# Kernel optimization log

Hardware: AMD Instinct MI355X
Metric: run time of the kernel (lower is better)

The kernel has to match this reference:

```python
import jax, jax.numpy as jnp
import numpy as np

B, L, H2 = 64, 1024, 1024  # batch, src_len, 2*hidden_size


def setup_inputs() -> dict:
    key = jax.random.key(0)
    k1, k2, k3, k4, k5, k6 = jax.random.split(key, 6)
    s = 0.02
    return {
        "s_t_hat": jax.random.normal(k1, (B, H2), jnp.float32),
        "encoder_outputs": jax.random.normal(k2, (B, L, H2), jnp.float32),
        "encoder_features": jax.random.normal(k3, (B * L, H2), jnp.float32),
        "encoder_pad_mask": jnp.ones((B, L), jnp.float32),
        "W": jax.random.normal(k4, (H2, H2), jnp.float32) * s,  # W_s_b_attn.weight
        "b": jax.random.normal(k5, (H2,), jnp.float32) * s,     # W_s_b_attn.bias
        "v": jax.random.normal(k6, (H2,), jnp.float32) * s,     # v.weight (no bias)
    }


def reference(s_t_hat, encoder_outputs, encoder_features, encoder_pad_mask, W, b, v):
    Bb, Ll, Hh = encoder_outputs.shape
    # decoder_features = W_s_b_attn(s_t_hat), broadcast over src positions
    dec = s_t_hat @ W.T + b                                # [B, H2]
    attn_feats = encoder_features.reshape(Bb, Ll, Hh) + dec[:, None, :]
    e = jnp.tanh(attn_feats) @ v                            # [B, L]
    attn_dist = jax.nn.softmax(e, axis=1) * encoder_pad_mask
    attn_dist = attn_dist / attn_dist.sum(axis=1, keepdims=True)
    c_t = jnp.einsum('bl,blh->bh', attn_dist, encoder_outputs)  # [B, H2]
    return c_t
```

## Files before the change

### kernel.cpp

```cpp
#include <hip/hip_runtime.h>

#define H2    1024
#define LSRC  1024
#define BATCH 64
#define NCH   32
#define CH    32
#define RPW   8

__device__ __forceinline__ float fast_tanh(float x) {
  float e2 = __expf(2.0f * x);
  return 1.0f - 2.0f * __builtin_amdgcn_rcpf(e2 + 1.0f);
}

__global__ __launch_bounds__(256) void dec_kernel(
    const float* __restrict__ s, const float* __restrict__ W,
    const float* __restrict__ bias, float* __restrict__ dec) {
  const int KT = 128;
  __shared__ float s_lds[BATCH][KT + 1];
  __shared__ float w_lds[16][KT];
  const int t  = threadIdx.x;
  const int h0 = blockIdx.x * 16;
  const int bi = t & 63;
  const int hg = t >> 6;
  float acc[4] = {0.f, 0.f, 0.f, 0.f};
  for (int k0 = 0; k0 < H2; k0 += KT) {
    __syncthreads();
    for (int idx = t; idx < BATCH * KT; idx += 256) {
      int r = idx >> 7, c = idx & (KT - 1);
      s_lds[r][c] = s[r * H2 + k0 + c];
    }
    for (int idx = t; idx < 16 * KT; idx += 256) {
      int r = idx >> 7, c = idx & (KT - 1);
      w_lds[r][c] = W[(h0 + r) * H2 + k0 + c];
    }
    __syncthreads();
    for (int k = 0; k < KT; ++k) {
      float sv = s_lds[bi][k];
#pragma unroll
      for (int j = 0; j < 4; ++j) acc[j] += sv * w_lds[hg + 4 * j][k];
    }
  }
#pragma unroll
  for (int j = 0; j < 4; ++j) {
    int h = h0 + hg + 4 * j;
    dec[bi * H2 + h] = acc[j] + bias[h];
  }
}

__global__ __launch_bounds__(256) void fused_kernel(
    const float* __restrict__ ef, const float* __restrict__ eo,
    const float* __restrict__ dec, const float* __restrict__ v,
    const float* __restrict__ mask, float* __restrict__ part,
    float* __restrict__ sums) {
  __shared__ float dv_lds[2 * H2];
  __shared__ float a_lds[CH];
  __shared__ float wpsum[4];
  const int t    = threadIdx.x;
  const int lane = t & 63;
  const int wave = t >> 6;
  const int lc   = blockIdx.x;
  const int b    = blockIdx.y;
  const int l0   = lc * CH;

  ((float4*)dv_lds)[t]       = ((const float4*)(dec + (size_t)b * H2))[t];
  ((float4*)dv_lds)[256 + t] = ((const float4*)v)[t];
  __syncthreads();

  const float4* efb = (const float4*)(ef) + ((size_t)b * LSRC + l0) * 256;
  float lsum = 0.f;
#pragma unroll
  for (int i = 0; i < RPW; ++i) {
    const int rl = wave + 4 * i;
    const float4* row = efb + (size_t)rl * 256;
    float sum = 0.f;
#pragma unroll
    for (int j = 0; j < 4; ++j) {
      float4 x  = row[lane + 64 * j];
      float4 dj = ((const float4*)dv_lds)[lane + 64 * j];
      float4 vj = ((const float4*)dv_lds)[256 + lane + 64 * j];
      sum += fast_tanh(x.x + dj.x) * vj.x;
      sum += fast_tanh(x.y + dj.y) * vj.y;
      sum += fast_tanh(x.z + dj.z) * vj.z;
      sum += fast_tanh(x.w + dj.w) * vj.w;
    }
#pragma unroll
    for (int off = 32; off; off >>= 1) sum += __shfl_xor(sum, off);
    float mk = mask[b * LSRC + l0 + rl];
    if (lane == 0) {
      float w = __expf(fminf(sum, 80.f)) * mk;
      a_lds[rl] = w;
      lsum += w;
    }
  }
  if (lane == 0) wpsum[wave] = lsum;
  __syncthreads();
  if (t == 0) sums[b * NCH + lc] = wpsum[0] + wpsum[1] + wpsum[2] + wpsum[3];

  const float4* eob = (const float4*)(eo) + ((size_t)b * LSRC + l0) * 256;
  float4 acc = {0.f, 0.f, 0.f, 0.f};
#pragma unroll 8
  for (int l = 0; l < CH; ++l) {
    float  a = a_lds[l];
    float4 x = eob[(size_t)l * 256 + t];
    acc.x += a * x.x; acc.y += a * x.y; acc.z += a * x.z; acc.w += a * x.w;
  }
  ((float4*)(part) + (size_t)(lc * BATCH + b) * 256)[t] = acc;
}

__global__ __launch_bounds__(256) void reduce_kernel(
    const float* __restrict__ part, const float* __restrict__ sums,
    float* __restrict__ out) {
  const int b = blockIdx.x, t = threadIdx.x;
  float Z = 0.f;
#pragma unroll
  for (int lc = 0; lc < NCH; ++lc) Z += sums[b * NCH + lc];
  float inv = 1.0f / Z;
  float4 s = {0.f, 0.f, 0.f, 0.f};
#pragma unroll
  for (int lc = 0; lc < NCH; ++lc) {
    float4 x = ((const float4*)(part) + (size_t)(lc * BATCH + b) * 256)[t];
    s.x += x.x; s.y += x.y; s.z += x.z; s.w += x.w;
  }
  float4 o = {s.x * inv, s.y * inv, s.z * inv, s.w * inv};
  ((float4*)(out) + (size_t)b * 256)[t] = o;
}

extern "C" void kernel_launch(void* const* d_in, const int* in_sizes, int n_in,
                              void* d_out, int out_size, void* d_ws, size_t ws_size,
                              hipStream_t stream) {
  const float* s_t_hat  = (const float*)d_in[0];
  const float* enc_out  = (const float*)d_in[1];
  const float* enc_feat = (const float*)d_in[2];
  const float* mask     = (const float*)d_in[3];
  const float* W        = (const float*)d_in[4];
  const float* bias     = (const float*)d_in[5];
  const float* v        = (const float*)d_in[6];
  float* out = (float*)d_out;

  float* dec  = (float*)d_ws;
  float* sums = dec + BATCH * H2;
  float* part = sums + BATCH * NCH;

  dec_kernel<<<H2 / 16, 256, 0, stream>>>(s_t_hat, W, bias, dec);
  fused_kernel<<<dim3(NCH, BATCH), 256, 0, stream>>>(
      enc_feat, enc_out, dec, v, mask, part, sums);
  reduce_kernel<<<BATCH, 256, 0, stream>>>(part, sums, out);
}
```

Measured before the change: 153.6 us.

## Reassign score computation: each thread owns a hidden slice across all rows with transpose-reduce

The score phase now has each thread hold a fixed float4 slice of dec and v in registers and compute partial tanh-dot products for all 32 rows. It then uses a butterfly transpose-reduction across lanes, so each lane ends up with one row's sum, and combines waves through shared memory. This replaces per-row full-wave shuffle reductions and the LDS staging of dec and v, and issues all 32 row loads up front for more memory-level parallelism. The cost is a 32-float register array, with launch bounds set to 4 blocks per SM to limit register pressure. The final weighted sum over encoder outputs is also fully unrolled.

```diff
diff --git a/kernel.cpp b/kernel.cpp
--- a/kernel.cpp
+++ b/kernel.cpp
@@ -5,7 +5,6 @@
 #define BATCH 64
 #define NCH   32
 #define CH    32
-#define RPW   8
 
 __device__ __forceinline__ float fast_tanh(float x) {
   float e2 = __expf(2.0f * x);
@@ -47,14 +46,13 @@
   }
 }
 
-__global__ __launch_bounds__(256) void fused_kernel(
+__global__ __launch_bounds__(256, 4) void fused_kernel(
     const float* __restrict__ ef, const float* __restrict__ eo,
     const float* __restrict__ dec, const float* __restrict__ v,
     const float* __restrict__ mask, float* __restrict__ part,
     float* __restrict__ sums) {
-  __shared__ float dv_lds[2 * H2];
+  __shared__ float apart[4][32];
   __shared__ float a_lds[CH];
-  __shared__ float wpsum[4];
   const int t    = threadIdx.x;
   const int lane = t & 63;
   const int wave = t >> 6;
@@ -62,47 +60,51 @@
   const int b    = blockIdx.y;
   const int l0   = lc * CH;
 
-  ((float4*)dv_lds)[t]       = ((const float4*)(dec + (size_t)b * H2))[t];
-  ((float4*)dv_lds)[256 + t] = ((const float4*)v)[t];
+  const int hq = wave * 64 + lane;
+  float4 dj = ((const float4*)(dec + (size_t)b * H2))[hq];
+  float4 vj = ((const float4*)v)[hq];
+
+  const float4* efb = (const float4*)(ef) + ((size_t)b * LSRC + l0) * 256 + hq;
+  float a[CH];
+#pragma unroll
+  for (int r = 0; r < CH; ++r) {
+    float4 x = efb[(size_t)r * 256];
+    a[r] = fast_tanh(x.x + dj.x) * vj.x + fast_tanh(x.y + dj.y) * vj.y +
+           fast_tanh(x.z + dj.z) * vj.z + fast_tanh(x.w + dj.w) * vj.w;
+  }
+#pragma unroll
+  for (int m = 32; m >= 2; m >>= 1) {
+    const int nh = m >> 1;
+    const bool hi = (lane & m) != 0;
+#pragma unroll
+    for (int r = 0; r < nh; ++r) {
+      float send = hi ? a[r] : a[r + nh];
+      float recv = __shfl_xor(send, m);
+      a[r] = (hi ? a[r + nh] : a[r]) + recv;
+    }
+  }
+  a[0] += __shfl_xor(a[0], 1);
+  if (!(lane & 1)) apart[wave][lane >> 1] = a[0];
   __syncthreads();
 
-  const float4* efb = (const float4*)(ef) + ((size_t)b * LSRC + l0) * 256;
-  float lsum = 0.f;
+  float wv = 0.f;
+  if (t < 32) {
+    float es = apart[0][t] + apart[1][t] + apart[2][t] + apart[3][t];
+    wv = __expf(fminf(es, 80.f)) * mask[b * LSRC + l0 + t];
+    a_lds[t] = wv;
+  }
 #pragma unroll
-  for (int i = 0; i < RPW; ++i) {
-    const int rl = wave + 4 * i;
-    const float4* row = efb + (size_t)rl * 256;
-    float sum = 0.f;
-#pragma unroll
-    for (int j = 0; j < 4; ++j) {
-      float4 x  = row[lane + 64 * j];
-      float4 dj = ((const float4*)dv_lds)[lane + 64 * j];
-      float4 vj = ((const float4*)dv_lds)[256 + lane + 64 * j];
-      sum += fast_tanh(x.x + dj.x) * vj.x;
-      sum += fast_tanh(x.y + dj.y) * vj.y;
-      sum += fast_tanh(x.z + dj.z) * vj.z;
-      sum += fast_tanh(x.w + dj.w) * vj.w;
-    }
-#pragma unroll
-    for (int off = 32; off; off >>= 1) sum += __shfl_xor(sum, off);
-    float mk = mask[b * LSRC + l0 + rl];
-    if (lane == 0) {
-      float w = __expf(fminf(sum, 80.f)) * mk;
-      a_lds[rl] = w;
-      lsum += w;
-    }
-  }
-  if (lane == 0) wpsum[wave] = lsum;
+  for (int off = 32; off >= 1; off >>= 1) wv += __shfl_xor(wv, off);
+  if (t == 0) sums[b * NCH + lc] = wv;
   __syncthreads();
-  if (t == 0) sums[b * NCH + lc] = wpsum[0] + wpsum[1] + wpsum[2] + wpsum[3];
 
   const float4* eob = (const float4*)(eo) + ((size_t)b * LSRC + l0) * 256;
   float4 acc = {0.f, 0.f, 0.f, 0.f};
-#pragma unroll 8
+#pragma unroll
   for (int l = 0; l < CH; ++l) {
-    float  a = a_lds[l];
-    float4 x = eob[(size_t)l * 256 + t];
-    acc.x += a * x.x; acc.y += a * x.y; acc.z += a * x.z; acc.w += a * x.w;
+    float  av = a_lds[l];
+    float4 x  = eob[(size_t)l * 256 + t];
+    acc.x += av * x.x; acc.y += av * x.y; acc.z += av * x.z; acc.w += av * x.w;
   }
   ((float4*)(part) + (size_t)(lc * BATCH + b) * 256)[t] = acc;
 }
```

After: 164.9 us. 1.07x slower.

## Split fused attention kernel into separate score and context kernels with strided rows

Applied to the files above, without the earlier changes.

Splits the fused score and context kernel into two kernels. e_kernel computes the unnormalized exp scores into a global buffer, striding each wave over rows across the whole batch and issuing all row and dec loads up front. ct_kernel then does the weighted sum of encoder_outputs with interleaved row slices, and the reduce kernel recomputes the normalizer from the score buffer. The aim is more memory-level parallelism and fewer serialized phases within each block, at the cost of an extra launch and a global round-trip for the weights.

```diff
diff --git a/kernel.cpp b/kernel.cpp
--- a/kernel.cpp
+++ b/kernel.cpp
@@ -3,9 +3,6 @@
 #define H2    1024
 #define LSRC  1024
 #define BATCH 64
-#define NCH   32
-#define CH    32
-#define RPW   8
 
 __device__ __forceinline__ float fast_tanh(float x) {
   float e2 = __expf(2.0f * x);
@@ -47,78 +44,91 @@
   }
 }
 
-__global__ __launch_bounds__(256) void fused_kernel(
-    const float* __restrict__ ef, const float* __restrict__ eo,
-    const float* __restrict__ dec, const float* __restrict__ v,
-    const float* __restrict__ mask, float* __restrict__ part,
-    float* __restrict__ sums) {
-  __shared__ float dv_lds[2 * H2];
-  __shared__ float a_lds[CH];
-  __shared__ float wpsum[4];
+__global__ __launch_bounds__(256, 4) void e_kernel(
+    const float* __restrict__ ef, const float* __restrict__ dec,
+    const float* __restrict__ v, const float* __restrict__ mask,
+    float* __restrict__ wbuf) {
+  __shared__ float v_lds[H2];
   const int t    = threadIdx.x;
   const int lane = t & 63;
   const int wave = t >> 6;
-  const int lc   = blockIdx.x;
-  const int b    = blockIdx.y;
-  const int l0   = lc * CH;
+  const int gw   = blockIdx.x * 4 + wave;
 
-  ((float4*)dv_lds)[t]       = ((const float4*)(dec + (size_t)b * H2))[t];
-  ((float4*)dv_lds)[256 + t] = ((const float4*)v)[t];
+  ((float4*)v_lds)[t] = ((const float4*)v)[t];
   __syncthreads();
+  float4 vv0 = ((const float4*)v_lds)[lane];
+  float4 vv1 = ((const float4*)v_lds)[lane + 64];
+  float4 vv2 = ((const float4*)v_lds)[lane + 128];
+  float4 vv3 = ((const float4*)v_lds)[lane + 192];
 
-  const float4* efb = (const float4*)(ef) + ((size_t)b * LSRC + l0) * 256;
-  float lsum = 0.f;
 #pragma unroll
-  for (int i = 0; i < RPW; ++i) {
-    const int rl = wave + 4 * i;
-    const float4* row = efb + (size_t)rl * 256;
+  for (int k = 0; k < 8; ++k) {
+    const int r = gw + 8192 * k;
+    const int b = r >> 10;
+    const float4* row  = (const float4*)(ef) + (size_t)r * 256 + lane;
+    const float4* dec4 = (const float4*)(dec) + (size_t)b * 256 + lane;
+    float4 x0 = row[0],    x1 = row[64],   x2 = row[128],  x3 = row[192];
+    float4 d0 = dec4[0],   d1 = dec4[64],  d2 = dec4[128], d3 = dec4[192];
     float sum = 0.f;
-#pragma unroll
-    for (int j = 0; j < 4; ++j) {
-      float4 x  = row[lane + 64 * j];
-      float4 dj = ((const float4*)dv_lds)[lane + 64 * j];
-      float4 vj = ((const float4*)dv_lds)[256 + lane + 64 * j];
-      sum += fast_tanh(x.x + dj.x) * vj.x;
-      sum += fast_tanh(x.y + dj.y) * vj.y;
-      sum += fast_tanh(x.z + dj.z) * vj.z;
-      sum += fast_tanh(x.w + dj.w) * vj.w;
-    }
+    sum += fast_tanh(x0.x + d0.x) * vv0.x + fast_tanh(x0.y + d0.y) * vv0.y +
+           fast_tanh(x0.z + d0.z) * vv0.z + fast_tanh(x0.w + d0.w) * vv0.w;
+    sum += fast_tanh(x1.x + d1.x) * vv1.x + fast_tanh(x1.y + d1.y) * vv1.y +
+           fast_tanh(x1.z + d1.z) * vv1.z + fast_tanh(x1.w + d1.w) * vv1.w;
+    sum += fast_tanh(x2.x + d2.x) * vv2.x + fast_tanh(x2.y + d2.y) * vv2.y +
+           fast_tanh(x2.z + d2.z) * vv2.z + fast_tanh(x2.w + d2.w) * vv2.w;
+    sum += fast_tanh(x3.x + d3.x) * vv3.x + fast_tanh(x3.y + d3.y) * vv3.y +
+           fast_tanh(x3.z + d3.z) * vv3.z + fast_tanh(x3.w + d3.w) * vv3.w;
 #pragma unroll
     for (int off = 32; off; off >>= 1) sum += __shfl_xor(sum, off);
-    float mk = mask[b * LSRC + l0 + rl];
-    if (lane == 0) {
-      float w = __expf(fminf(sum, 80.f)) * mk;
-      a_lds[rl] = w;
-      lsum += w;
-    }
+    float mk = mask[r];
+    if (lane == 0) wbuf[r] = __expf(fminf(sum, 80.f)) * mk;
   }
-  if (lane == 0) wpsum[wave] = lsum;
-  __syncthreads();
-  if (t == 0) sums[b * NCH + lc] = wpsum[0] + wpsum[1] + wpsum[2] + wpsum[3];
+}
 
-  const float4* eob = (const float4*)(eo) + ((size_t)b * LSRC + l0) * 256;
+__global__ __launch_bounds__(256, 4) void ct_kernel(
+    const float* __restrict__ eo, const float* __restrict__ wbuf,
+    float* __restrict__ part) {
+  const int t  = threadIdx.x;
+  const int b  = blockIdx.x >> 5;
+  const int lb = blockIdx.x & 31;
+  const float4* eob = (const float4*)(eo) + ((size_t)b * LSRC + lb) * 256 + t;
+  const float*  wb  = wbuf + b * LSRC + lb;
   float4 acc = {0.f, 0.f, 0.f, 0.f};
-#pragma unroll 8
-  for (int l = 0; l < CH; ++l) {
-    float  a = a_lds[l];
-    float4 x = eob[(size_t)l * 256 + t];
-    acc.x += a * x.x; acc.y += a * x.y; acc.z += a * x.z; acc.w += a * x.w;
+#pragma unroll
+  for (int k = 0; k < 32; k += 4) {
+    float  w0 = wb[32 * k];
+    float  w1 = wb[32 * (k + 1)];
+    float  w2 = wb[32 * (k + 2)];
+    float  w3 = wb[32 * (k + 3)];
+    float4 x0 = eob[(size_t)(32 * k) * 256];
+    float4 x1 = eob[(size_t)(32 * (k + 1)) * 256];
+    float4 x2 = eob[(size_t)(32 * (k + 2)) * 256];
+    float4 x3 = eob[(size_t)(32 * (k + 3)) * 256];
+    acc.x += w0 * x0.x; acc.y += w0 * x0.y; acc.z += w0 * x0.z; acc.w += w0 * x0.w;
+    acc.x += w1 * x1.x; acc.y += w1 * x1.y; acc.z += w1 * x1.z; acc.w += w1 * x1.w;
+    acc.x += w2 * x2.x; acc.y += w2 * x2.y; acc.z += w2 * x2.z; acc.w += w2 * x2.w;
+    acc.x += w3 * x3.x; acc.y += w3 * x3.y; acc.z += w3 * x3.z; acc.w += w3 * x3.w;
   }
-  ((float4*)(part) + (size_t)(lc * BATCH + b) * 256)[t] = acc;
+  ((float4*)(part))[(size_t)blockIdx.x * 256 + t] = acc;
 }
 
 __global__ __launch_bounds__(256) void reduce_kernel(
-    const float* __restrict__ part, const float* __restrict__ sums,
+    const float* __restrict__ part, const float* __restrict__ wbuf,
     float* __restrict__ out) {
+  __shared__ float wsum[4];
   const int b = blockIdx.x, t = threadIdx.x;
-  float Z = 0.f;
+  const int lane = t & 63, wave = t >> 6;
+  float4 wv = ((const float4*)(wbuf + b * LSRC))[t];
+  float z = wv.x + wv.y + wv.z + wv.w;
 #pragma unroll
-  for (int lc = 0; lc < NCH; ++lc) Z += sums[b * NCH + lc];
-  float inv = 1.0f / Z;
+  for (int off = 32; off; off >>= 1) z += __shfl_xor(z, off);
+  if (lane == 0) wsum[wave] = z;
+  __syncthreads();
+  float inv = 1.0f / (wsum[0] + wsum[1] + wsum[2] + wsum[3]);
   float4 s = {0.f, 0.f, 0.f, 0.f};
 #pragma unroll
-  for (int lc = 0; lc < NCH; ++lc) {
-    float4 x = ((const float4*)(part) + (size_t)(lc * BATCH + b) * 256)[t];
+  for (int lb = 0; lb < 32; ++lb) {
+    float4 x = ((const float4*)(part))[(size_t)(b * 32 + lb) * 256 + t];
     s.x += x.x; s.y += x.y; s.z += x.z; s.w += x.w;
   }
   float4 o = {s.x * inv, s.y * inv, s.z * inv, s.w * inv};
@@ -138,11 +148,11 @@
   float* out = (float*)d_out;
 
   float* dec  = (float*)d_ws;
-  float* sums = dec + BATCH * H2;
-  float* part = sums + BATCH * NCH;
+  float* wbuf = dec + BATCH * H2;
+  float* part = wbuf + BATCH * LSRC;
 
   dec_kernel<<<H2 / 16, 256, 0, stream>>>(s_t_hat, W, bias, dec);
-  fused_kernel<<<dim3(NCH, BATCH), 256, 0, stream>>>(
-      enc_feat, enc_out, dec, v, mask, part, sums);
-  reduce_kernel<<<BATCH, 256, 0, stream>>>(part, sums, out);
+  e_kernel<<<2048, 256, 0, stream>>>(enc_feat, dec, v, mask, wbuf);
+  ct_kernel<<<2048, 256, 0, stream>>>(enc_out, wbuf, part);
+  reduce_kernel<<<BATCH, 256, 0, stream>>>(part, wbuf, out);
 }
```

After: 165.0 us. +7.4%, slower.
